# Performance work log

Measured on AMD Instinct MI355X. Metric: run time of the kernel, lower is better.

The kernel has to match this reference:

```python
import jax, jax.numpy as jnp
import numpy as np

POOL = 7
NUM_ROIS = 256
SCALE = 1.0 / 16.0  # feature-map stride
H, W, C = 128, 128, 1024
STRIDE = 16


def setup_inputs() -> dict:
    key = jax.random.key(0)
    k_img, k_wh, k_xy = jax.random.split(key, 3)
    img = jax.random.normal(k_img, (1, H, W, C), dtype=jnp.float32)
    # ROIs in image-pixel units (x, y, w, h); w,h >= 16 so crop >= 1 feature cell
    max_px = H * STRIDE  # 2048
    wh = jax.random.uniform(k_wh, (1, NUM_ROIS, 2), minval=16.0, maxval=max_px * 0.5)
    xy = jax.random.uniform(k_xy, (1, NUM_ROIS, 2), minval=0.0, maxval=1.0) * (max_px - wh)
    rois = jnp.concatenate([xy, wh], axis=-1).astype(jnp.float32)
    return {"img": img, "rois": rois}


def _pool_one_roi(img0, roi):
    # img0: (H, W, C); roi: (4,) = (x, y, w, h) in pixels.
    # Original: int cast of scaled coords, crop img[y:y+h, x:x+w],
    # then TF1 bilinear resize (align_corners=False, src = i * in/out).
    c = (roi * SCALE).astype(jnp.int32)  # truncation == floor for positive coords
    x0, y0, w, h = c[0], c[1], c[2], c[3]
    i = jnp.arange(POOL, dtype=jnp.float32)
    # source coords within the cropped section
    sy = i * (h.astype(jnp.float32) / POOL)
    sx = i * (w.astype(jnp.float32) / POOL)
    fy = jnp.floor(sy)
    fx = jnp.floor(sx)
    ty = sy - fy  # (P,) lerp weights
    tx = sx - fx
    y_lo = fy.astype(jnp.int32)
    x_lo = fx.astype(jnp.int32)
    y_hi = jnp.minimum(y_lo + 1, jnp.maximum(h - 1, 0))  # clamp at section edge
    x_hi = jnp.minimum(x_lo + 1, jnp.maximum(w - 1, 0))
    gy0 = jnp.clip(y0 + y_lo, 0, H - 1)
    gy1 = jnp.clip(y0 + y_hi, 0, H - 1)
    gx0 = jnp.clip(x0 + x_lo, 0, W - 1)
    gx1 = jnp.clip(x0 + x_hi, 0, W - 1)
    v00 = img0[gy0[:, None], gx0[None, :]]  # (P, P, C)
    v01 = img0[gy0[:, None], gx1[None, :]]
    v10 = img0[gy1[:, None], gx0[None, :]]
    v11 = img0[gy1[:, None], gx1[None, :]]
    top = v00 + tx[None, :, None] * (v01 - v00)
    bot = v10 + tx[None, :, None] * (v11 - v10)
    return top + ty[:, None, None] * (bot - top)  # (P, P, C)


def reference(img, rois):
    img0 = img[0]  # (H, W, C)
    pooled = jax.vmap(lambda r: _pool_one_roi(img0, r))(rois[0])  # (NR, P, P, C)
    return pooled[None]  # (1, num_rois, pool, pool, C)
```

## Files before the change

kernel.cpp:

```cpp
#include <hip/hip_runtime.h>


#define IMG_H 128
#define IMG_W 128
#define IMG_C 1024
#define POOLK 7
#define NROIS 256

typedef float vfloat4 __attribute__((ext_vector_type(4)));

__global__ __launch_bounds__(256) void roi_pool_kernel(
    const float* __restrict__ img,
    const float* __restrict__ rois,
    float* __restrict__ out) {
  const int iy = blockIdx.x;
  const int r  = blockIdx.y;

  const vfloat4 roi = *(const vfloat4*)(rois + (size_t)r * 4);

  const int x0 = (int)(roi.x * 0.0625f);
  const int y0 = (int)(roi.y * 0.0625f);
  const int w  = (int)(roi.z * 0.0625f);
  const int h  = (int)(roi.w * 0.0625f);

  const float sy = (float)iy * ((float)h / 7.0f);
  const float fy = floorf(sy);
  const float ty = sy - fy;
  const int y_lo = (int)fy;
  const int y_hi = min(y_lo + 1, max(h - 1, 0));
  const int gy0 = min(max(y0 + y_lo, 0), IMG_H - 1);
  const int gy1 = min(max(y0 + y_hi, 0), IMG_H - 1);

  const int c = threadIdx.x * 4;
  const float* row0 = img + (size_t)gy0 * (IMG_W * IMG_C) + c;
  const float* row1 = img + (size_t)gy1 * (IMG_W * IMG_C) + c;
  float* orow = out + (((size_t)r * POOLK + iy) * POOLK) * IMG_C + c;

  const float step_x = (float)w / 7.0f;
  const int xmax = max(w - 1, 0);

#pragma unroll
  for (int ix = 0; ix < POOLK; ++ix) {
    const float sx = (float)ix * step_x;
    const float fx = floorf(sx);
    const float tx = sx - fx;
    const int x_lo = (int)fx;
    const int x_hi = min(x_lo + 1, xmax);
    const int gx0 = min(max(x0 + x_lo, 0), IMG_W - 1);
    const int gx1 = min(max(x0 + x_hi, 0), IMG_W - 1);

    const vfloat4 v00 = *(const vfloat4*)(row0 + (size_t)gx0 * IMG_C);
    const vfloat4 v01 = *(const vfloat4*)(row0 + (size_t)gx1 * IMG_C);
    const vfloat4 v10 = *(const vfloat4*)(row1 + (size_t)gx0 * IMG_C);
    const vfloat4 v11 = *(const vfloat4*)(row1 + (size_t)gx1 * IMG_C);

    const vfloat4 top = v00 + tx * (v01 - v00);
    const vfloat4 bot = v10 + tx * (v11 - v10);
    const vfloat4 o   = top + ty * (bot - top);

    *(vfloat4*)(orow + (size_t)ix * IMG_C) = o;
  }
}

extern "C" void kernel_launch(void* const* d_in, const int* in_sizes, int n_in,
                              void* d_out, int out_size, void* d_ws, size_t ws_size,
                              hipStream_t stream) {
  const float* img  = (const float*)d_in[0];
  const float* rois = (const float*)d_in[1];
  float* out = (float*)d_out;

  dim3 grid(POOLK, NROIS);
  dim3 block(256);
  roi_pool_kernel<<<grid, block, 0, stream>>>(img, rois, out);
}
```

Measured before the change: 120.2 us.

## Skip redundant bilinear loads, remap blocks across XCDs, use nontemporal stores

Remaps the flat block index so consecutive blocks of the same ROI land on the same XCD, which should improve L2 reuse of gathered rows. Each corner load is skipped when its interpolation weight is zero or the high and low indices coincide, cutting global reads. Output stores become nontemporal to avoid polluting cache, and ROI values are made scalar with readfirstlane. It adds branches, although they are uniform across the block, and changes occupancy hints through launch bounds.

```diff
diff --git a/kernel.cpp b/kernel.cpp
--- a/kernel.cpp
+++ b/kernel.cpp
@@ -6,24 +6,29 @@
 #define IMG_C 1024
 #define POOLK 7
 #define NROIS 256
+#define NBLK (POOLK * NROIS)
+#define NXCD 8
+#define CHUNK (NBLK / NXCD)
 
 typedef float vfloat4 __attribute__((ext_vector_type(4)));
 
-__global__ __launch_bounds__(256) void roi_pool_kernel(
+__global__ __launch_bounds__(256, 8) void roi_pool_kernel(
     const float* __restrict__ img,
     const float* __restrict__ rois,
     float* __restrict__ out) {
-  const int iy = blockIdx.x;
-  const int r  = blockIdx.y;
+  const int orig = (int)blockIdx.x;
+  const int newb = (orig & (NXCD - 1)) * CHUNK + (orig >> 3);
+  const int r  = newb / POOLK;
+  const int iy = newb - r * POOLK;
 
   const vfloat4 roi = *(const vfloat4*)(rois + (size_t)r * 4);
 
-  const int x0 = (int)(roi.x * 0.0625f);
-  const int y0 = (int)(roi.y * 0.0625f);
-  const int w  = (int)(roi.z * 0.0625f);
-  const int h  = (int)(roi.w * 0.0625f);
+  const int x0 = __builtin_amdgcn_readfirstlane((int)(roi.x * 0.0625f));
+  const int y0 = __builtin_amdgcn_readfirstlane((int)(roi.y * 0.0625f));
+  const int w  = __builtin_amdgcn_readfirstlane((int)(roi.z * 0.0625f));
+  const int h  = __builtin_amdgcn_readfirstlane((int)(roi.w * 0.0625f));
 
-  const float sy = (float)iy * ((float)h / 7.0f);
+  const float sy = (float)iy * ((float)h * (1.0f / 7.0f));
   const float fy = floorf(sy);
   const float ty = sy - fy;
   const int y_lo = (int)fy;
@@ -31,12 +36,14 @@
   const int gy0 = min(max(y0 + y_lo, 0), IMG_H - 1);
   const int gy1 = min(max(y0 + y_hi, 0), IMG_H - 1);
 
-  const int c = threadIdx.x * 4;
+  const bool needY = (ty != 0.0f) && (gy1 != gy0);
+
+  const int c = (int)threadIdx.x * 4;
   const float* row0 = img + (size_t)gy0 * (IMG_W * IMG_C) + c;
   const float* row1 = img + (size_t)gy1 * (IMG_W * IMG_C) + c;
   float* orow = out + (((size_t)r * POOLK + iy) * POOLK) * IMG_C + c;
 
-  const float step_x = (float)w / 7.0f;
+  const float step_x = (float)w * (1.0f / 7.0f);
   const int xmax = max(w - 1, 0);
 
 #pragma unroll
@@ -48,17 +55,27 @@
     const int x_hi = min(x_lo + 1, xmax);
     const int gx0 = min(max(x0 + x_lo, 0), IMG_W - 1);
     const int gx1 = min(max(x0 + x_hi, 0), IMG_W - 1);
+    const bool needX = (tx != 0.0f) && (gx1 != gx0);
 
     const vfloat4 v00 = *(const vfloat4*)(row0 + (size_t)gx0 * IMG_C);
-    const vfloat4 v01 = *(const vfloat4*)(row0 + (size_t)gx1 * IMG_C);
-    const vfloat4 v10 = *(const vfloat4*)(row1 + (size_t)gx0 * IMG_C);
-    const vfloat4 v11 = *(const vfloat4*)(row1 + (size_t)gx1 * IMG_C);
+    vfloat4 top = v00;
+    if (needX) {
+      const vfloat4 v01 = *(const vfloat4*)(row0 + (size_t)gx1 * IMG_C);
+      top = v00 + tx * (v01 - v00);
+    }
 
-    const vfloat4 top = v00 + tx * (v01 - v00);
-    const vfloat4 bot = v10 + tx * (v11 - v10);
-    const vfloat4 o   = top + ty * (bot - top);
+    vfloat4 o = top;
+    if (needY) {
+      const vfloat4 v10 = *(const vfloat4*)(row1 + (size_t)gx0 * IMG_C);
+      vfloat4 bot = v10;
+      if (needX) {
+        const vfloat4 v11 = *(const vfloat4*)(row1 + (size_t)gx1 * IMG_C);
+        bot = v10 + tx * (v11 - v10);
+      }
+      o = top + ty * (bot - top);
+    }
 
-    *(vfloat4*)(orow + (size_t)ix * IMG_C) = o;
+    __builtin_nontemporal_store(o, (vfloat4*)(orow + (size_t)ix * IMG_C));
   }
 }
 
@@ -69,7 +86,7 @@
   const float* rois = (const float*)d_in[1];
   float* out = (float*)d_out;
 
-  dim3 grid(POOLK, NROIS);
+  dim3 grid(NBLK);
   dim3 block(256);
   roi_pool_kernel<<<grid, block, 0, stream>>>(img, rois, out);
 }
```

Result: no change. 118.8 us (-1.1%).
